# Performance work log

Hardware: AMD Instinct MI355X
Metric: run time of the kernel (lower is better)

Reference implementation:

```python
import jax, jax.numpy as jnp
from jax import lax
import numpy as np

SEARCH = 9          # search window (asserted == 9 in source)
PAD = SEARCH // 2   # 4
NUM_BINS = 10       # num_dist_bins
BIN_DISP = 0.5      # bin_displacement
NUM_ITER = 3        # num_iter
MIN_FILTER_REG = 1e-5


def _distance_map():
    # DistanceMap: soft-bin the radial distance from the window center.
    c = float(SEARCH // 2)
    yy, xx = jnp.meshgrid(jnp.arange(SEARCH, dtype=jnp.float32),
                          jnp.arange(SEARCH, dtype=jnp.float32), indexing='ij')
    d = jnp.sqrt((yy - c) ** 2 + (xx - c) ** 2) / BIN_DISP          # (9,9)
    k = jnp.arange(NUM_BINS, dtype=jnp.float32)
    bd = d[..., None] - k                                            # (9,9,B)
    vals = jnp.maximum(1.0 - jnp.abs(bd), 0.0)
    last = jnp.clip(bd[..., -1] + 1.0, 0.0, 1.0)                     # saturating last bin
    return vals.at[..., -1].set(last)                                # (9,9,B)


def _local_corr(f, ref_pad, disp):
    # f: (b,c,H,W); ref_pad: (b,c,H+8,W+8) -> scores (b,81,H,W)
    b, c, H, W = f.shape
    def step(_, d):
        r = lax.dynamic_slice(ref_pad, (0, 0, d[0], d[1]), (b, c, H, W))
        return None, jnp.einsum('bchw,bchw->bhw', f, r)
    _, out = lax.scan(step, None, disp)                              # (81,b,H,W)
    return jnp.moveaxis(out, 0, 1)


def _local_corr_t(res, ref_pad, disp):
    # res: (b,81,H,W) -> (b,c,H,W); adjoint of _local_corr w.r.t. the filter arg
    b, c = ref_pad.shape[0], ref_pad.shape[1]
    H, W = res.shape[2], res.shape[3]
    def step(acc, xs):
        d, rd = xs                                                   # rd: (b,H,W)
        r = lax.dynamic_slice(ref_pad, (0, 0, d[0], d[1]), (b, c, H, W))
        return acc + rd[:, None] * r, None
    acc0 = jnp.zeros((b, c, H, W), ref_pad.dtype)
    acc, _ = lax.scan(step, acc0, (disp, jnp.moveaxis(res, 1, 0)))
    return acc


def setup_inputs() -> dict:
    key = jax.random.key(0)
    k1, k2 = jax.random.split(key)
    b, c, H, W = 4, 128, 128, 128
    d = jnp.arange(NUM_BINS, dtype=jnp.float32) * BIN_DISP
    return {
        'filter_map': jax.random.normal(k1, (b, c, H, W), jnp.float32),
        'reference_feat': jax.random.normal(k2, (b, c, H, W), jnp.float32),
        # 1x1-conv predictor weights (num_bins -> 1), at their documented inits:
        'label_w': jnp.exp(-0.5 * d ** 2),            # init_gauss, sigma=1.0
        'spatial_w': jnp.ones((NUM_BINS,), jnp.float32),
        'mask_w': 4.0 * jnp.tanh(2.0 - d),            # v_minus_init_factor * tanh(2 - d)
        'log_step_length': jnp.zeros((1,), jnp.float32),   # log(1.0)
        'filter_reg': 0.01 * jnp.ones((1,), jnp.float32),
    }


def reference(filter_map, reference_feat, label_w, spatial_w, mask_w,
              log_step_length, filter_reg):
    b, c, H, W = filter_map.shape
    dm = _distance_map()                                             # (9,9,B)
    target_map = (dm @ label_w).reshape(1, SEARCH * SEARCH, 1, 1)
    v_plus = (dm @ spatial_w).reshape(1, SEARCH * SEARCH, 1, 1)
    weight_m = jax.nn.sigmoid(dm @ mask_w).reshape(1, SEARCH * SEARCH, 1, 1)

    step_length = jnp.exp(log_step_length).reshape(1, 1, 1, 1)
    reg_weight = jnp.maximum(filter_reg * filter_reg,
                             MIN_FILTER_REG ** 2).reshape(1, 1, 1, 1) / (c * c)

    dys, dxs = jnp.meshgrid(jnp.arange(SEARCH), jnp.arange(SEARCH), indexing='ij')
    disp = jnp.stack([dys.ravel(), dxs.ravel()], axis=1)             # (81,2)
    ref_pad = jnp.pad(reference_feat, ((0, 0), (0, 0), (PAD, PAD), (PAD, PAD)))

    # LeakyReluPar: f(s,a) = (1-a)/2*|s| + (1+a)/2*s ; deriv: (1-a)/2*sign(s) + (1+a)/2
    a_lo = (1.0 - weight_m) * 0.5
    a_hi = (1.0 + weight_m) * 0.5

    f = filter_map
    for _ in range(NUM_ITER):
        scores = _local_corr(f, ref_pad, disp)                       # (b,81,H,W)
        act = v_plus * (a_lo * jnp.abs(scores) + a_hi * scores)
        grad_act = v_plus * (a_lo * jnp.sign(scores) + a_hi)
        residuals = act - v_plus * target_map
        mapped = grad_act * residuals
        f_grad = reg_weight * f + _local_corr_t(mapped, ref_pad, disp)
        sg = grad_act * _local_corr(f_grad, ref_pad, disp)
        alpha_den = jnp.sum(sg * sg, axis=1, keepdims=True)          # (b,1,H,W)
        alpha_num = jnp.sum(f_grad * f_grad, axis=1, keepdims=True)
        alpha = alpha_num / jnp.maximum(alpha_den + reg_weight * alpha_num, 1e-8)
        f = f - step_length * alpha * f_grad
    return f
```

## Files before the change

### kernel.cpp

```cpp
#include <hip/hip_runtime.h>

#define BB 4
#define CC 128
#define HH 128
#define WW 128
#define HW (HH*WW)
#define CHW (CC*HW)
#define ND 81
#define CP 136
#define UPITCH 40
#define PP 32
#define SP 88

typedef short s8v __attribute__((ext_vector_type(8)));
typedef short s4v __attribute__((ext_vector_type(4)));
typedef float f4v __attribute__((ext_vector_type(4)));

__device__ __forceinline__ short f2bf(float x){
  unsigned u = __float_as_uint(x);
  unsigned r = (u + 0x7FFFu + ((u >> 16) & 1u)) >> 16;
  return (short)r;
}
__device__ __forceinline__ float bf2f(short s){
  return __uint_as_float(((unsigned)(unsigned short)s) << 16);
}

__global__ void coef_kernel(const float* lw, const float* sw, const float* mw,
                            const float* lsl, const float* fr, float* coef){
  int d = threadIdx.x;
  if (d < ND){
    float dy = (float)(d / 9) - 4.0f;
    float dx = (float)(d % 9) - 4.0f;
    float dist = sqrtf(dy*dy + dx*dx) * 2.0f;
    float t = 0.f, v = 0.f, m = 0.f;
    for (int k = 0; k < 10; k++){
      float bd = dist - (float)k;
      float val = (k == 9) ? fminf(fmaxf(bd + 1.0f, 0.f), 1.f)
                           : fmaxf(1.0f - fabsf(bd), 0.f);
      t += val * lw[k]; v += val * sw[k]; m += val * mw[k];
    }
    float wm = 1.f / (1.f + expf(-m));
    coef[d] = t; coef[128+d] = v;
    coef[256+d] = (1.f - wm) * 0.5f;
    coef[384+d] = (1.f + wm) * 0.5f;
  }
  if (threadIdx.x == 0){
    coef[512] = expf(lsl[0]);
    float f = fr[0];
    coef[513] = fmaxf(f*f, 1e-10f) / (float)(CC*CC);
  }
}

__global__ __launch_bounds__(256)
void cvt_kernel(const float* ref, short* refT, short* refU){
  __shared__ short T[128*130];
  int r = blockIdx.x, bb = blockIdx.y;
  int tid = threadIdx.x;
  const float* src = ref + (size_t)bb*CHW + (size_t)r*WW;
  short* uout = refU + (size_t)(bb*HH + r) * CC * WW;
  short* tout = refT + (size_t)(bb*HH + r) * WW * CC;
  #pragma unroll
  for (int k = 0; k < 16; k++){
    int q = tid + (k << 8);
    int c = q >> 5, u0 = (q & 31) * 4;
    float4 v = *(const float4*)(src + (size_t)c*HW + u0);
    short h0 = f2bf(v.x), h1 = f2bf(v.y), h2 = f2bf(v.z), h3 = f2bf(v.w);
    s4v pk = {h0, h1, h2, h3};
    *(s4v*)&uout[(size_t)c*WW + u0] = pk;
    T[c*130 + u0 + 0] = h0; T[c*130 + u0 + 1] = h1;
    T[c*130 + u0 + 2] = h2; T[c*130 + u0 + 3] = h3;
  }
  __syncthreads();
  #pragma unroll
  for (int k = 0; k < 16; k++){
    int o = tid + (k << 8);
    int u = o >> 5, c0 = (o & 31) * 4;
    s4v pk = {T[(c0+0)*130 + u], T[(c0+1)*130 + u],
              T[(c0+2)*130 + u], T[(c0+3)*130 + u]};
    *(s4v*)&tout[(size_t)u*CC + c0] = pk;
  }
}

#define L_UC   0
#define L_FGS  8704
#define L_CU   8704
#define L_PM   18944
#define L_CF   26112
#define L_SGN  27648
#define L_DEN  33280
#define L_NUM  33536
#define L_SA   33792
#define L_SZ   34048

template<int PRE>
__global__ __launch_bounds__(256, 4)
void kF(const float* f_in, const float* ref, const short* refT, const short* refU,
        const float* coef, float* f_out){
  __shared__ char smem[L_SZ];
  short* uc  = (short*)(smem + L_UC);
  short* cu  = (short*)(smem + L_CU);
  short* Pm  = (short*)(smem + L_PM);
  short* fgs = (short*)(smem + L_FGS);
  float* s_t = (float*)(smem + L_CF);
  float* s_v = s_t + 96; float* s_al = s_t + 192; float* s_ah = s_t + 288;
  signed char* sgn = (signed char*)(smem + L_SGN);
  float* den = (float*)(smem + L_DEN);
  float* num = (float*)(smem + L_NUM);
  float* sa  = (float*)(smem + L_SA);

  int tid = threadIdx.x;
  int lane = tid & 63, wv = tid >> 6;
  int quad = lane >> 4, col = lane & 15;

  int hwid = blockIdx.x + (blockIdx.y << 3) + (blockIdx.z << 8);
  int virt = ((hwid & 7) << 7) + (hwid >> 3);
  int bb = virt >> 8, y0 = ((virt >> 3) & 31) * 4, x0 = (virt & 7) * 16;

  int ub = x0 - 8;

  const float* fimg = f_in + (size_t)bb * CHW;
  const float* rimg = ref  + (size_t)bb * CHW;

  if (tid < ND){
    s_t[tid]  = coef[tid];       s_v[tid]  = coef[128+tid];
    s_al[tid] = coef[256+tid];   s_ah[tid] = coef[384+tid];
  }

  s8v pT0, pT1, pU0, pU1;
  float4 pF0, pF1, pF2, pF3;

  auto loadT = [&](int r){
    if constexpr (PRE){
      const short* tb = refT + (size_t)(bb*HH + r) * WW * CC;
      { int e = tid;       int ua = ub + (e >> 4);
        pT0 = (ua >= 0 && ua < WW)
              ? *(const s8v*)(tb + (size_t)ua*CC + ((e & 15) << 3)) : (s8v)(short)0; }
      { int e = tid + 256; int ua = ub + (e >> 4);
        pT1 = (ua >= 0 && ua < WW)
              ? *(const s8v*)(tb + (size_t)ua*CC + ((e & 15) << 3)) : (s8v)(short)0; }
    } else {
      const float* rb = rimg + (size_t)r * WW;
      float4 z; z.x = z.y = z.z = z.w = 0.f;
      { int e = tid;       int ua = ub + (e & 7)*4;
        pF0 = (ua >= 0 && ua + 4 <= WW) ? *(const float4*)(rb + (size_t)(e >> 3)*HW + ua) : z; }
      { int e = tid + 256; int ua = ub + (e & 7)*4;
        pF1 = (ua >= 0 && ua + 4 <= WW) ? *(const float4*)(rb + (size_t)(e >> 3)*HW + ua) : z; }
      { int e = tid + 512; int ua = ub + (e & 7)*4;
        pF2 = (ua >= 0 && ua + 4 <= WW) ? *(const float4*)(rb + (size_t)(e >> 3)*HW + ua) : z; }
      { int e = tid + 768; int ua = ub + (e & 7)*4;
        pF3 = (ua >= 0 && ua + 4 <= WW) ? *(const float4*)(rb + (size_t)(e >> 3)*HW + ua) : z; }
    }
  };
  auto loadU = [&](int r){
    if constexpr (PRE){
      const short* ubp = refU + (size_t)(bb*HH + r) * CC * WW;
      { int e = tid;       int ua = ub + ((e & 3) << 3);
        pU0 = (ua >= 0 && ua + 8 <= WW)
              ? *(const s8v*)(ubp + (size_t)(e >> 2)*WW + ua) : (s8v)(short)0; }
      { int e = tid + 256; int ua = ub + ((e & 3) << 3);
        pU1 = (ua >= 0 && ua + 8 <= WW)
              ? *(const s8v*)(ubp + (size_t)(e >> 2)*WW + ua) : (s8v)(short)0; }
    }
  };
  auto writeRowA = [&](){
    if constexpr (PRE){
      { int e = tid;       *(s8v*)&uc[(e >> 4)*CP + ((e & 15) << 3)] = pT0; }
      { int e = tid + 256; *(s8v*)&uc[(e >> 4)*CP + ((e & 15) << 3)] = pT1; }
      { int e = tid;       *(s8v*)&cu[(e >> 2)*UPITCH + ((e & 3) << 3)] = pU0; }
      { int e = tid + 256; *(s8v*)&cu[(e >> 2)*UPITCH + ((e & 3) << 3)] = pU1; }
    } else {
      float4 vv[4] = {pF0, pF1, pF2, pF3};
      #pragma unroll
      for (int k = 0; k < 4; k++){
        int e4 = tid + (k << 8);
        int u4 = (e4 & 7) * 4, c = e4 >> 3;
        short h0 = f2bf(vv[k].x), h1 = f2bf(vv[k].y),
              h2 = f2bf(vv[k].z), h3 = f2bf(vv[k].w);
        uc[(u4+0)*CP + c] = h0; uc[(u4+1)*CP + c] = h1;
        uc[(u4+2)*CP + c] = h2; uc[(u4+3)*CP + c] = h3;
        s4v pk = {h0, h1, h2, h3};
        *(s4v*)&cu[c*UPITCH + u4] = pk;
      }
    }
  };
  auto writeRowB = [&](){
    if constexpr (PRE){
      { int e = tid;       *(s8v*)&uc[(e >> 4)*CP + ((e & 15) << 3)] = pT0; }
      { int e = tid + 256; *(s8v*)&uc[(e >> 4)*CP + ((e & 15) << 3)] = pT1; }
    } else {
      float4 vv[4] = {pF0, pF1, pF2, pF3};
      #pragma unroll
      for (int k = 0; k < 4; k++){
        int e4 = tid + (k << 8);
        int u4 = (e4 & 7) * 4, c = e4 >> 3;
        uc[(u4+0)*CP + c] = f2bf(vv[k].x); uc[(u4+1)*CP + c] = f2bf(vv[k].y);
        uc[(u4+2)*CP + c] = f2bf(vv[k].z); uc[(u4+3)*CP + c] = f2bf(vv[k].w);
      }
    }
  };

  if (y0 - 4 >= 0){ loadT(y0 - 4); loadU(y0 - 4); }

  int fy = y0 + wv;
  s8v a_hi[4], a_lo[4];
  #pragma unroll
  for (int kc = 0; kc < 4; kc++){
    short th[8], tl[8];
    #pragma unroll
    for (int j = 0; j < 8; j++){
      int c = kc*32 + quad*8 + j;
      float v = fimg[(size_t)c * HW + fy * WW + x0 + col];
      short h = f2bf(v);
      th[j] = h; tl[j] = f2bf(v - bf2f(h));
    }
    a_hi[kc] = *(const s8v*)th;
    a_lo[kc] = *(const s8v*)tl;
  }

  f4v D[8];
  #pragma unroll
  for (int i = 0; i < 8; i++) D[i] = (f4v)0.f;

  for (int rr = 0; rr < 12; rr++){
    int r = y0 + rr - 4;
    bool rv = (r >= 0) && (r < HH);
    __syncthreads();
    if (rv) writeRowA();
    __syncthreads();
    if (rr < 11){
      int rn = r + 1;
      if (rn >= 0 && rn < HH){ loadT(rn); loadU(rn); }
    }
    int dy = rr - wv;
    if (rv && dy >= 0 && dy <= 8){
      f4v C0 = (f4v)0.f, C1 = (f4v)0.f;
      #pragma unroll
      for (int kc = 0; kc < 4; kc++){
        s8v b0 = *(const s8v*)&uc[col*CP      + kc*32 + quad*8];
        s8v b1 = *(const s8v*)&uc[(16+col)*CP + kc*32 + quad*8];
        C0 = __builtin_amdgcn_mfma_f32_16x16x32_bf16(a_hi[kc], b0, C0, 0,0,0);
        C0 = __builtin_amdgcn_mfma_f32_16x16x32_bf16(a_lo[kc], b0, C0, 0,0,0);
        C1 = __builtin_amdgcn_mfma_f32_16x16x32_bf16(a_hi[kc], b1, C1, 0,0,0);
        C1 = __builtin_amdgcn_mfma_f32_16x16x32_bf16(a_lo[kc], b1, C1, 0,0,0);
      }
      #pragma unroll
      for (int nt = 0; nt < 2; nt++){
        f4v Cv = nt ? C1 : C0;
        #pragma unroll
        for (int reg = 0; reg < 4; reg++){
          int x  = quad*4 + reg;
          int up = nt*16 + col;
          int dxm = up - x - 4;
          float m = 0.f;
          if (dxm >= 0 && dxm <= 8){
            float s = Cv[reg];
            int d = dy*9 + dxm;
            int px = wv*16 + x;
            signed char sc = (s > 0.f) ? (signed char)1
                           : ((s < 0.f) ? (signed char)-1 : (signed char)0);
            sgn[px*SP + d] = sc;
            float sgf = (float)sc;
            float vp = s_v[d], al = s_al[d], ah = s_ah[d];
            float ga  = vp * (al * sgf + ah);
            float act = vp * (al * fabsf(s) + ah * s);
            m = ga * (act - vp * s_t[d]);
          }
          Pm[(wv*16 + x)*PP + up] = f2bf(m);
        }
      }
      asm volatile("s_waitcnt lgkmcnt(0)" ::: "memory");
      __builtin_amdgcn_sched_barrier(0);
      s8v pa = *(const s8v*)&Pm[(wv*16 + col)*PP + quad*8];
      #pragma unroll
      for (int ct = 0; ct < 8; ct++){
        s8v bc = *(const s8v*)&cu[(ct*16 + col)*UPITCH + quad*8];
        D[ct] = __builtin_amdgcn_mfma_f32_16x16x32_bf16(pa, bc, D[ct], 0,0,0);
      }
    }
  }

  if (y0 - 4 >= 0) loadT(y0 - 4);

  float rw = coef[513];
  __syncthreads();
  #pragma unroll
  for (int ct = 0; ct < 8; ct++){
    #pragma unroll
    for (int reg = 0; reg < 4; reg++){
      int x = quad*4 + reg, c = ct*16 + col;
      float fv = fimg[(size_t)c * HW + fy * WW + x0 + x];
      fgs[(wv*16 + x)*CP + c] = f2bf(D[ct][reg] + rw * fv);
    }
  }
  __syncthreads();
  if (tid < 64){
    float s = 0.f;
    #pragma unroll
    for (int kc = 0; kc < 16; kc++){
      s8v v = *(const s8v*)&fgs[tid*CP + kc*8];
      #pragma unroll
      for (int j = 0; j < 8; j++){ float f = bf2f(v[j]); s += f*f; }
    }
    num[tid] = s;
  }

  s8v ga_[4];
  #pragma unroll
  for (int kc = 0; kc < 4; kc++)
    ga_[kc] = *(const s8v*)&fgs[(wv*16 + col)*CP + kc*32 + quad*8];

  float dacc[4] = {0.f, 0.f, 0.f, 0.f};

  for (int rr = 0; rr < 12; rr++){
    int r = y0 + rr - 4;
    bool rv = (r >= 0) && (r < HH);
    __syncthreads();
    if (rv) writeRowB();
    __syncthreads();
    if (rr < 11){
      int rn = r + 1;
      if (rn >= 0 && rn < HH) loadT(rn);
    }
    int dy = rr - wv;
    if (rv && dy >= 0 && dy <= 8){
      f4v C0 = (f4v)0.f, C1 = (f4v)0.f;
      #pragma unroll
      for (int kc = 0; kc < 4; kc++){
        s8v b0 = *(const s8v*)&uc[col*CP      + kc*32 + quad*8];
        s8v b1 = *(const s8v*)&uc[(16+col)*CP + kc*32 + quad*8];
        C0 = __builtin_amdgcn_mfma_f32_16x16x32_bf16(ga_[kc], b0, C0, 0,0,0);
        C1 = __builtin_amdgcn_mfma_f32_16x16x32_bf16(ga_[kc], b1, C1, 0,0,0);
      }
      #pragma unroll
      for (int nt = 0; nt < 2; nt++){
        f4v Cv = nt ? C1 : C0;
        #pragma unroll
        for (int reg = 0; reg < 4; reg++){
          int x  = quad*4 + reg;
          int up = nt*16 + col;
          int dxm = up - x - 4;
          if (dxm >= 0 && dxm <= 8){
            int d = dy*9 + dxm;
            int px = wv*16 + x;
            float sgf = (float)sgn[px*SP + d];
            float ga = s_v[d] * (s_al[d]*sgf + s_ah[d]);
            float t  = Cv[reg];
            float sgv = ga * t;
            dacc[reg] += sgv*sgv;
          }
        }
      }
    }
  }

  #pragma unroll
  for (int reg = 0; reg < 4; reg++){
    float v = dacc[reg];
    v += __shfl_xor(v, 1);
    v += __shfl_xor(v, 2);
    v += __shfl_xor(v, 4);
    v += __shfl_xor(v, 8);
    if (col == 0) den[wv*16 + quad*4 + reg] = v;
  }

  __syncthreads();
  if (tid < 64){
    float step = coef[512];
    float alpha = num[tid] / fmaxf(den[tid] + rw*num[tid], 1e-8f);
    sa[tid] = step * alpha;
  }
  __syncthreads();

  float* oimg = f_out + (size_t)bb * CHW;
  for (int e = tid; e < 8192; e += 256){
    int x = e & 15, y = (e >> 4) & 3, c = e >> 6;
    size_t gi = (size_t)c * HW + (y0 + y) * WW + x0 + x;
    float v = fimg[gi] - sa[y*16 + x] * bf2f(fgs[(y*16 + x)*CP + c]);
    oimg[gi] = v;
  }
}

extern "C" void kernel_launch(void* const* d_in, const int* in_sizes, int n_in,
                              void* d_out, int out_size, void* d_ws, size_t ws_size,
                              hipStream_t stream) {
  const float* filter_map = (const float*)d_in[0];
  const float* ref        = (const float*)d_in[1];
  const float* label_w    = (const float*)d_in[2];
  const float* spatial_w  = (const float*)d_in[3];
  const float* mask_w     = (const float*)d_in[4];
  const float* lsl        = (const float*)d_in[5];
  const float* freg       = (const float*)d_in[6];

  float* coef = (float*)d_ws;
  float* fbuf = (float*)d_out;

  short* refT = (short*)((char*)d_ws + 65536);
  short* refU = refT + (size_t)BB * CHW;
  size_t need = 65536 + 2 * (size_t)BB * CHW * sizeof(short);
  bool pre = (ws_size >= need);

  coef_kernel<<<dim3(1), dim3(128), 0, stream>>>(label_w, spatial_w, mask_w, lsl, freg, coef);
  if (pre)
    cvt_kernel<<<dim3(HH, BB), dim3(256), 0, stream>>>(ref, refT, refU);

  dim3 grid(8, 32, BB);
  for (int it = 0; it < 3; it++){
    const float* fsrc = (it == 0) ? filter_map : (const float*)fbuf;
    if (pre) kF<1><<<grid, 256, 0, stream>>>(fsrc, ref, refT, refU, coef, fbuf);
    else     kF<0><<<grid, 256, 0, stream>>>(fsrc, ref, refT, refU, coef, fbuf);
  }
}
```

Baseline: 351.7 us.

## Double-buffer reference rows, keep score signs in registers, fold activation coefficients

Row staging buffers in shared memory become double-buffered, so each iteration needs one barrier instead of two, and the next row is written while the current one is computed. Score signs move from a shared-memory byte array into packed 64-bit shift registers carried from the first sweep to the second. The per-displacement coefficients are pre-combined into three sign-selected gradient factors plus v*t, which simplifies the per-element math. The larger shared footprint drops launch bounds from 4 to 3 blocks per CU, trading occupancy for fewer syncs.

```diff
diff --git a/kernel.cpp b/kernel.cpp
--- a/kernel.cpp
+++ b/kernel.cpp
@@ -10,7 +10,8 @@
 #define CP 136
 #define UPITCH 40
 #define PP 32
-#define SP 88
+#define UCSZ (32*CP)
+#define CUSZ (128*UPITCH)
 
 typedef short s8v __attribute__((ext_vector_type(8)));
 typedef short s4v __attribute__((ext_vector_type(4)));
@@ -40,9 +41,10 @@
       t += val * lw[k]; v += val * sw[k]; m += val * mw[k];
     }
     float wm = 1.f / (1.f + expf(-m));
-    coef[d] = t; coef[128+d] = v;
-    coef[256+d] = (1.f - wm) * 0.5f;
-    coef[384+d] = (1.f + wm) * 0.5f;
+    coef[d]     = v;
+    coef[96+d]  = v * wm;
+    coef[192+d] = v * (1.f + wm) * 0.5f;
+    coef[288+d] = v * t;
   }
   if (threadIdx.x == 0){
     coef[512] = expf(lsl[0]);
@@ -82,18 +84,17 @@
 }
 
 #define L_UC   0
-#define L_FGS  8704
-#define L_CU   8704
-#define L_PM   18944
-#define L_CF   26112
-#define L_SGN  27648
-#define L_DEN  33280
-#define L_NUM  33536
-#define L_SA   33792
-#define L_SZ   34048
+#define L_CU   17408
+#define L_FGS  17408
+#define L_PM   37888
+#define L_CF   41984
+#define L_DEN  43520
+#define L_NUM  43776
+#define L_SA   44032
+#define L_SZ   44288
 
 template<int PRE>
-__global__ __launch_bounds__(256, 4)
+__global__ __launch_bounds__(256, 3)
 void kF(const float* f_in, const float* ref, const short* refT, const short* refU,
         const float* coef, float* f_out){
   __shared__ char smem[L_SZ];
@@ -101,9 +102,9 @@
   short* cu  = (short*)(smem + L_CU);
   short* Pm  = (short*)(smem + L_PM);
   short* fgs = (short*)(smem + L_FGS);
-  float* s_t = (float*)(smem + L_CF);
-  float* s_v = s_t + 96; float* s_al = s_t + 192; float* s_ah = s_t + 288;
-  signed char* sgn = (signed char*)(smem + L_SGN);
+  float* s_cf = (float*)(smem + L_CF);
+  float* s_vp = s_cf; float* s_vpwm = s_cf + 96;
+  float* s_vpah = s_cf + 192; float* s_vpt = s_cf + 288;
   float* den = (float*)(smem + L_DEN);
   float* num = (float*)(smem + L_NUM);
   float* sa  = (float*)(smem + L_SA);
@@ -120,11 +121,6 @@
 
   const float* fimg = f_in + (size_t)bb * CHW;
   const float* rimg = ref  + (size_t)bb * CHW;
-
-  if (tid < ND){
-    s_t[tid]  = coef[tid];       s_v[tid]  = coef[128+tid];
-    s_al[tid] = coef[256+tid];   s_ah[tid] = coef[384+tid];
-  }
 
   s8v pT0, pT1, pU0, pU1;
   float4 pF0, pF1, pF2, pF3;
@@ -162,12 +158,13 @@
               ? *(const s8v*)(ubp + (size_t)(e >> 2)*WW + ua) : (s8v)(short)0; }
     }
   };
-  auto writeRowA = [&](){
+  auto writeRowA = [&](int b){
+    short* ucb = uc + b*UCSZ; short* cub = cu + b*CUSZ;
     if constexpr (PRE){
-      { int e = tid;       *(s8v*)&uc[(e >> 4)*CP + ((e & 15) << 3)] = pT0; }
-      { int e = tid + 256; *(s8v*)&uc[(e >> 4)*CP + ((e & 15) << 3)] = pT1; }
-      { int e = tid;       *(s8v*)&cu[(e >> 2)*UPITCH + ((e & 3) << 3)] = pU0; }
-      { int e = tid + 256; *(s8v*)&cu[(e >> 2)*UPITCH + ((e & 3) << 3)] = pU1; }
+      { int e = tid;       *(s8v*)&ucb[(e >> 4)*CP + ((e & 15) << 3)] = pT0; }
+      { int e = tid + 256; *(s8v*)&ucb[(e >> 4)*CP + ((e & 15) << 3)] = pT1; }
+      { int e = tid;       *(s8v*)&cub[(e >> 2)*UPITCH + ((e & 3) << 3)] = pU0; }
+      { int e = tid + 256; *(s8v*)&cub[(e >> 2)*UPITCH + ((e & 3) << 3)] = pU1; }
     } else {
       float4 vv[4] = {pF0, pF1, pF2, pF3};
       #pragma unroll
@@ -176,30 +173,33 @@
         int u4 = (e4 & 7) * 4, c = e4 >> 3;
         short h0 = f2bf(vv[k].x), h1 = f2bf(vv[k].y),
               h2 = f2bf(vv[k].z), h3 = f2bf(vv[k].w);
-        uc[(u4+0)*CP + c] = h0; uc[(u4+1)*CP + c] = h1;
-        uc[(u4+2)*CP + c] = h2; uc[(u4+3)*CP + c] = h3;
+        ucb[(u4+0)*CP + c] = h0; ucb[(u4+1)*CP + c] = h1;
+        ucb[(u4+2)*CP + c] = h2; ucb[(u4+3)*CP + c] = h3;
         s4v pk = {h0, h1, h2, h3};
-        *(s4v*)&cu[c*UPITCH + u4] = pk;
+        *(s4v*)&cub[c*UPITCH + u4] = pk;
       }
     }
   };
-  auto writeRowB = [&](){
+  auto writeRowB = [&](int b){
+    short* ucb = uc + b*UCSZ;
     if constexpr (PRE){
-      { int e = tid;       *(s8v*)&uc[(e >> 4)*CP + ((e & 15) << 3)] = pT0; }
-      { int e = tid + 256; *(s8v*)&uc[(e >> 4)*CP + ((e & 15) << 3)] = pT1; }
+      { int e = tid;       *(s8v*)&ucb[(e >> 4)*CP + ((e & 15) << 3)] = pT0; }
+      { int e = tid + 256; *(s8v*)&ucb[(e >> 4)*CP + ((e & 15) << 3)] = pT1; }
     } else {
       float4 vv[4] = {pF0, pF1, pF2, pF3};
       #pragma unroll
       for (int k = 0; k < 4; k++){
         int e4 = tid + (k << 8);
         int u4 = (e4 & 7) * 4, c = e4 >> 3;
-        uc[(u4+0)*CP + c] = f2bf(vv[k].x); uc[(u4+1)*CP + c] = f2bf(vv[k].y);
-        uc[(u4+2)*CP + c] = f2bf(vv[k].z); uc[(u4+3)*CP + c] = f2bf(vv[k].w);
+        ucb[(u4+0)*CP + c] = f2bf(vv[k].x); ucb[(u4+1)*CP + c] = f2bf(vv[k].y);
+        ucb[(u4+2)*CP + c] = f2bf(vv[k].z); ucb[(u4+3)*CP + c] = f2bf(vv[k].w);
       }
     }
   };
 
   if (y0 - 4 >= 0){ loadT(y0 - 4); loadU(y0 - 4); }
+
+  for (int e = tid; e < 384; e += 256) s_cf[e] = coef[e];
 
   int fy = y0 + wv;
   s8v a_hi[4], a_lo[4];
@@ -221,61 +221,67 @@
   #pragma unroll
   for (int i = 0; i < 8; i++) D[i] = (f4v)0.f;
 
+  unsigned long long f0 = 0ull, f1 = 0ull, f2 = 0ull;
+
+  if (y0 - 4 >= 0) writeRowA(0);
+  if (y0 - 3 >= 0){ loadT(y0 - 3); loadU(y0 - 3); }
+
   for (int rr = 0; rr < 12; rr++){
     int r = y0 + rr - 4;
     bool rv = (r >= 0) && (r < HH);
     __syncthreads();
-    if (rv) writeRowA();
-    __syncthreads();
-    if (rr < 11){
-      int rn = r + 1;
-      if (rn >= 0 && rn < HH){ loadT(rn); loadU(rn); }
-    }
+    if (rr < 11 && r + 1 >= 0 && r + 1 < HH) writeRowA((rr + 1) & 1);
+    if (rr < 10 && r + 2 >= 0 && r + 2 < HH){ loadT(r + 2); loadU(r + 2); }
     int dy = rr - wv;
-    if (rv && dy >= 0 && dy <= 8){
-      f4v C0 = (f4v)0.f, C1 = (f4v)0.f;
-      #pragma unroll
-      for (int kc = 0; kc < 4; kc++){
-        s8v b0 = *(const s8v*)&uc[col*CP      + kc*32 + quad*8];
-        s8v b1 = *(const s8v*)&uc[(16+col)*CP + kc*32 + quad*8];
-        C0 = __builtin_amdgcn_mfma_f32_16x16x32_bf16(a_hi[kc], b0, C0, 0,0,0);
-        C0 = __builtin_amdgcn_mfma_f32_16x16x32_bf16(a_lo[kc], b0, C0, 0,0,0);
-        C1 = __builtin_amdgcn_mfma_f32_16x16x32_bf16(a_hi[kc], b1, C1, 0,0,0);
-        C1 = __builtin_amdgcn_mfma_f32_16x16x32_bf16(a_lo[kc], b1, C1, 0,0,0);
-      }
-      #pragma unroll
-      for (int nt = 0; nt < 2; nt++){
-        f4v Cv = nt ? C1 : C0;
+    if (dy >= 0 && dy <= 8){
+      unsigned pack = 0u;
+      if (rv){
+        const short* ucb = uc + (rr & 1)*UCSZ;
+        const short* cub = cu + (rr & 1)*CUSZ;
+        f4v C0 = (f4v)0.f, C1 = (f4v)0.f;
         #pragma unroll
-        for (int reg = 0; reg < 4; reg++){
-          int x  = quad*4 + reg;
-          int up = nt*16 + col;
-          int dxm = up - x - 4;
-          float m = 0.f;
-          if (dxm >= 0 && dxm <= 8){
-            float s = Cv[reg];
-            int d = dy*9 + dxm;
-            int px = wv*16 + x;
-            signed char sc = (s > 0.f) ? (signed char)1
-                           : ((s < 0.f) ? (signed char)-1 : (signed char)0);
-            sgn[px*SP + d] = sc;
-            float sgf = (float)sc;
-            float vp = s_v[d], al = s_al[d], ah = s_ah[d];
-            float ga  = vp * (al * sgf + ah);
-            float act = vp * (al * fabsf(s) + ah * s);
-            m = ga * (act - vp * s_t[d]);
+        for (int kc = 0; kc < 4; kc++){
+          s8v b0 = *(const s8v*)&ucb[col*CP      + kc*32 + quad*8];
+          s8v b1 = *(const s8v*)&ucb[(16+col)*CP + kc*32 + quad*8];
+          C0 = __builtin_amdgcn_mfma_f32_16x16x32_bf16(a_hi[kc], b0, C0, 0,0,0);
+          C0 = __builtin_amdgcn_mfma_f32_16x16x32_bf16(a_lo[kc], b0, C0, 0,0,0);
+          C1 = __builtin_amdgcn_mfma_f32_16x16x32_bf16(a_hi[kc], b1, C1, 0,0,0);
+          C1 = __builtin_amdgcn_mfma_f32_16x16x32_bf16(a_lo[kc], b1, C1, 0,0,0);
+        }
+        #pragma unroll
+        for (int nt = 0; nt < 2; nt++){
+          f4v Cv = nt ? C1 : C0;
+          #pragma unroll
+          for (int reg = 0; reg < 4; reg++){
+            int x  = quad*4 + reg;
+            int up = nt*16 + col;
+            int dxm = up - x - 4;
+            float m = 0.f;
+            if ((unsigned)dxm <= 8u){
+              float s = Cv[reg];
+              int d = dy*9 + dxm;
+              unsigned pos = (s > 0.f) ? 1u : 0u;
+              unsigned neg = (s < 0.f) ? 1u : 0u;
+              const float* gap = pos ? s_vp : (neg ? s_vpwm : s_vpah);
+              float ga = gap[d];
+              m = ga * (ga * s - s_vpt[d]);
+              pack |= (pos | (neg << 1)) << ((nt*4 + reg) * 2);
+            }
+            Pm[(wv*16 + x)*PP + up] = f2bf(m);
           }
-          Pm[(wv*16 + x)*PP + up] = f2bf(m);
+        }
+        asm volatile("s_waitcnt lgkmcnt(0)" ::: "memory");
+        __builtin_amdgcn_sched_barrier(0);
+        s8v pa = *(const s8v*)&Pm[(wv*16 + col)*PP + quad*8];
+        #pragma unroll
+        for (int ct = 0; ct < 8; ct++){
+          s8v bc = *(const s8v*)&cub[(ct*16 + col)*UPITCH + quad*8];
+          D[ct] = __builtin_amdgcn_mfma_f32_16x16x32_bf16(pa, bc, D[ct], 0,0,0);
         }
       }
-      asm volatile("s_waitcnt lgkmcnt(0)" ::: "memory");
-      __builtin_amdgcn_sched_barrier(0);
-      s8v pa = *(const s8v*)&Pm[(wv*16 + col)*PP + quad*8];
-      #pragma unroll
-      for (int ct = 0; ct < 8; ct++){
-        s8v bc = *(const s8v*)&cu[(ct*16 + col)*UPITCH + quad*8];
-        D[ct] = __builtin_amdgcn_mfma_f32_16x16x32_bf16(pa, bc, D[ct], 0,0,0);
-      }
+      f0 = (f0 >> 16) | (f1 << 48);
+      f1 = (f1 >> 16) | (f2 << 48);
+      f2 = (f2 >> 16) | ((unsigned long long)pack << 48);
     }
   }
 
@@ -309,44 +315,49 @@
   for (int kc = 0; kc < 4; kc++)
     ga_[kc] = *(const s8v*)&fgs[(wv*16 + col)*CP + kc*32 + quad*8];
 
+  if (y0 - 4 >= 0) writeRowB(0);
+  if (y0 - 3 >= 0) loadT(y0 - 3);
+
   float dacc[4] = {0.f, 0.f, 0.f, 0.f};
 
   for (int rr = 0; rr < 12; rr++){
     int r = y0 + rr - 4;
     bool rv = (r >= 0) && (r < HH);
     __syncthreads();
-    if (rv) writeRowB();
-    __syncthreads();
-    if (rr < 11){
-      int rn = r + 1;
-      if (rn >= 0 && rn < HH) loadT(rn);
-    }
+    if (rr < 11 && r + 1 >= 0 && r + 1 < HH) writeRowB((rr + 1) & 1);
+    if (rr < 10 && r + 2 >= 0 && r + 2 < HH) loadT(r + 2);
     int dy = rr - wv;
-    if (rv && dy >= 0 && dy <= 8){
-      f4v C0 = (f4v)0.f, C1 = (f4v)0.f;
-      #pragma unroll
-      for (int kc = 0; kc < 4; kc++){
-        s8v b0 = *(const s8v*)&uc[col*CP      + kc*32 + quad*8];
-        s8v b1 = *(const s8v*)&uc[(16+col)*CP + kc*32 + quad*8];
-        C0 = __builtin_amdgcn_mfma_f32_16x16x32_bf16(ga_[kc], b0, C0, 0,0,0);
-        C1 = __builtin_amdgcn_mfma_f32_16x16x32_bf16(ga_[kc], b1, C1, 0,0,0);
-      }
-      #pragma unroll
-      for (int nt = 0; nt < 2; nt++){
-        f4v Cv = nt ? C1 : C0;
+    if (dy >= 0 && dy <= 8){
+      unsigned pack = (unsigned)(f0 >> 48) & 0xFFFFu;
+      f0 = (f0 >> 16) | (f1 << 48);
+      f1 = (f1 >> 16) | (f2 << 48);
+      f2 >>= 16;
+      if (rv){
+        const short* ucb = uc + (rr & 1)*UCSZ;
+        f4v C0 = (f4v)0.f, C1 = (f4v)0.f;
         #pragma unroll
-        for (int reg = 0; reg < 4; reg++){
-          int x  = quad*4 + reg;
-          int up = nt*16 + col;
-          int dxm = up - x - 4;
-          if (dxm >= 0 && dxm <= 8){
-            int d = dy*9 + dxm;
-            int px = wv*16 + x;
-            float sgf = (float)sgn[px*SP + d];
-            float ga = s_v[d] * (s_al[d]*sgf + s_ah[d]);
-            float t  = Cv[reg];
-            float sgv = ga * t;
-            dacc[reg] += sgv*sgv;
+        for (int kc = 0; kc < 4; kc++){
+          s8v b0 = *(const s8v*)&ucb[col*CP      + kc*32 + quad*8];
+          s8v b1 = *(const s8v*)&ucb[(16+col)*CP + kc*32 + quad*8];
+          C0 = __builtin_amdgcn_mfma_f32_16x16x32_bf16(ga_[kc], b0, C0, 0,0,0);
+          C1 = __builtin_amdgcn_mfma_f32_16x16x32_bf16(ga_[kc], b1, C1, 0,0,0);
+        }
+        #pragma unroll
+        for (int nt = 0; nt < 2; nt++){
+          f4v Cv = nt ? C1 : C0;
+          #pragma unroll
+          for (int reg = 0; reg < 4; reg++){
+            int x  = quad*4 + reg;
+            int up = nt*16 + col;
+            int dxm = up - x - 4;
+            if ((unsigned)dxm <= 8u){
+              int d = dy*9 + dxm;
+              unsigned b2 = pack >> ((nt*4 + reg) * 2);
+              const float* gap = (b2 & 1u) ? s_vp : ((b2 & 2u) ? s_vpwm : s_vpah);
+              float ga = gap[d];
+              float sgv = ga * Cv[reg];
+              dacc[reg] += sgv*sgv;
+            }
           }
         }
       }
```

Result: slower. 388.0 us (+10.3%).

## Precompute sign-indexed coefficient tables and keep score signs in registers

Applied to the files above, without the earlier changes.

The coefficient kernel now precomputes, for each of the three score-sign cases, the squared gradient factor and its product with the target. The residual-times-gradient term therefore collapses to a single fma, and the denominator term uses one table lookup. The per-pixel sign array in shared memory is removed. The signs are packed as 2-bit fields into three 64-bit registers that shift like a queue from the first pass to the second, which cuts LDS traffic and shared-memory footprint. The cost is extra register pressure, plus reliance on the shift sequence of both loops matching exactly.

```diff
diff --git a/kernel.cpp b/kernel.cpp
--- a/kernel.cpp
+++ b/kernel.cpp
@@ -10,7 +10,6 @@
 #define CP 136
 #define UPITCH 40
 #define PP 32
-#define SP 88
 
 typedef short s8v __attribute__((ext_vector_type(8)));
 typedef short s4v __attribute__((ext_vector_type(4)));
@@ -40,14 +39,20 @@
       t += val * lw[k]; v += val * sw[k]; m += val * mw[k];
     }
     float wm = 1.f / (1.f + expf(-m));
-    coef[d] = t; coef[128+d] = v;
-    coef[256+d] = (1.f - wm) * 0.5f;
-    coef[384+d] = (1.f + wm) * 0.5f;
+    float ah = (1.f + wm) * 0.5f;
+    float gp = v, gn = v * wm, gz = v * ah;
+    float vt = v * t;
+    coef[d]       = gp * gp;
+    coef[96+d]    = gn * gn;
+    coef[192+d]   = gz * gz;
+    coef[288+d]   = gp * vt;
+    coef[384+d]   = gn * vt;
+    coef[480+d]   = gz * vt;
   }
   if (threadIdx.x == 0){
-    coef[512] = expf(lsl[0]);
+    coef[576] = expf(lsl[0]);
     float f = fr[0];
-    coef[513] = fmaxf(f*f, 1e-10f) / (float)(CC*CC);
+    coef[577] = fmaxf(f*f, 1e-10f) / (float)(CC*CC);
   }
 }
 
@@ -86,11 +91,10 @@
 #define L_CU   8704
 #define L_PM   18944
 #define L_CF   26112
-#define L_SGN  27648
-#define L_DEN  33280
-#define L_NUM  33536
-#define L_SA   33792
-#define L_SZ   34048
+#define L_DEN  28672
+#define L_NUM  28928
+#define L_SA   29184
+#define L_SZ   29440
 
 template<int PRE>
 __global__ __launch_bounds__(256, 4)
@@ -101,9 +105,9 @@
   short* cu  = (short*)(smem + L_CU);
   short* Pm  = (short*)(smem + L_PM);
   short* fgs = (short*)(smem + L_FGS);
-  float* s_t = (float*)(smem + L_CF);
-  float* s_v = s_t + 96; float* s_al = s_t + 192; float* s_ah = s_t + 288;
-  signed char* sgn = (signed char*)(smem + L_SGN);
+  float* s_cf = (float*)(smem + L_CF);
+  float* s_g2 = s_cf;
+  float* s_gt = s_cf + 288;
   float* den = (float*)(smem + L_DEN);
   float* num = (float*)(smem + L_NUM);
   float* sa  = (float*)(smem + L_SA);
@@ -120,11 +124,6 @@
 
   const float* fimg = f_in + (size_t)bb * CHW;
   const float* rimg = ref  + (size_t)bb * CHW;
-
-  if (tid < ND){
-    s_t[tid]  = coef[tid];       s_v[tid]  = coef[128+tid];
-    s_al[tid] = coef[256+tid];   s_ah[tid] = coef[384+tid];
-  }
 
   s8v pT0, pT1, pU0, pU1;
   float4 pF0, pF1, pF2, pF3;
@@ -201,6 +200,8 @@
 
   if (y0 - 4 >= 0){ loadT(y0 - 4); loadU(y0 - 4); }
 
+  for (int e = tid; e < 640; e += 256) s_cf[e] = coef[e];
+
   int fy = y0 + wv;
   s8v a_hi[4], a_lo[4];
   #pragma unroll
@@ -220,6 +221,8 @@
   f4v D[8];
   #pragma unroll
   for (int i = 0; i < 8; i++) D[i] = (f4v)0.f;
+
+  unsigned long long f0 = 0ull, f1 = 0ull, f2 = 0ull;
 
   for (int rr = 0; rr < 12; rr++){
     int r = y0 + rr - 4;
@@ -232,56 +235,60 @@
       if (rn >= 0 && rn < HH){ loadT(rn); loadU(rn); }
     }
     int dy = rr - wv;
-    if (rv && dy >= 0 && dy <= 8){
-      f4v C0 = (f4v)0.f, C1 = (f4v)0.f;
-      #pragma unroll
-      for (int kc = 0; kc < 4; kc++){
-        s8v b0 = *(const s8v*)&uc[col*CP      + kc*32 + quad*8];
-        s8v b1 = *(const s8v*)&uc[(16+col)*CP + kc*32 + quad*8];
-        C0 = __builtin_amdgcn_mfma_f32_16x16x32_bf16(a_hi[kc], b0, C0, 0,0,0);
-        C0 = __builtin_amdgcn_mfma_f32_16x16x32_bf16(a_lo[kc], b0, C0, 0,0,0);
-        C1 = __builtin_amdgcn_mfma_f32_16x16x32_bf16(a_hi[kc], b1, C1, 0,0,0);
-        C1 = __builtin_amdgcn_mfma_f32_16x16x32_bf16(a_lo[kc], b1, C1, 0,0,0);
-      }
-      #pragma unroll
-      for (int nt = 0; nt < 2; nt++){
-        f4v Cv = nt ? C1 : C0;
+    if (dy >= 0 && dy <= 8){
+      unsigned pack = 0u;
+      if (rv){
+        f4v C0 = (f4v)0.f, C1 = (f4v)0.f;
         #pragma unroll
-        for (int reg = 0; reg < 4; reg++){
-          int x  = quad*4 + reg;
-          int up = nt*16 + col;
-          int dxm = up - x - 4;
-          float m = 0.f;
-          if (dxm >= 0 && dxm <= 8){
-            float s = Cv[reg];
-            int d = dy*9 + dxm;
-            int px = wv*16 + x;
-            signed char sc = (s > 0.f) ? (signed char)1
-                           : ((s < 0.f) ? (signed char)-1 : (signed char)0);
-            sgn[px*SP + d] = sc;
-            float sgf = (float)sc;
-            float vp = s_v[d], al = s_al[d], ah = s_ah[d];
-            float ga  = vp * (al * sgf + ah);
-            float act = vp * (al * fabsf(s) + ah * s);
-            m = ga * (act - vp * s_t[d]);
+        for (int kc = 0; kc < 4; kc++){
+          s8v b0 = *(const s8v*)&uc[col*CP      + kc*32 + quad*8];
+          s8v b1 = *(const s8v*)&uc[(16+col)*CP + kc*32 + quad*8];
+          C0 = __builtin_amdgcn_mfma_f32_16x16x32_bf16(a_hi[kc], b0, C0, 0,0,0);
+          C0 = __builtin_amdgcn_mfma_f32_16x16x32_bf16(a_lo[kc], b0, C0, 0,0,0);
+          C1 = __builtin_amdgcn_mfma_f32_16x16x32_bf16(a_hi[kc], b1, C1, 0,0,0);
+          C1 = __builtin_amdgcn_mfma_f32_16x16x32_bf16(a_lo[kc], b1, C1, 0,0,0);
+        }
+        #pragma unroll
+        for (int nt = 0; nt < 2; nt++){
+          f4v Cv = nt ? C1 : C0;
+          #pragma unroll
+          for (int reg = 0; reg < 4; reg++){
+            int x  = quad*4 + reg;
+            int up = nt*16 + col;
+            int dxm = up - x - 4;
+            float m = 0.f;
+            if ((unsigned)dxm <= 8u){
+              float s = Cv[reg];
+              int d = dy*9 + dxm;
+              unsigned pos = (s > 0.f) ? 1u : 0u;
+              unsigned neg = (s < 0.f) ? 1u : 0u;
+              int off = pos ? 0 : (neg ? 96 : 192);
+              float g2 = s_g2[off + d];
+              float gt = s_gt[off + d];
+              m = fmaf(g2, s, -gt);
+              pack |= (pos | (neg << 1)) << ((nt*4 + reg) * 2);
+            }
+            Pm[(wv*16 + x)*PP + up] = f2bf(m);
           }
-          Pm[(wv*16 + x)*PP + up] = f2bf(m);
+        }
+        asm volatile("s_waitcnt lgkmcnt(0)" ::: "memory");
+        __builtin_amdgcn_sched_barrier(0);
+        s8v pa = *(const s8v*)&Pm[(wv*16 + col)*PP + quad*8];
+        #pragma unroll
+        for (int ct = 0; ct < 8; ct++){
+          s8v bc = *(const s8v*)&cu[(ct*16 + col)*UPITCH + quad*8];
+          D[ct] = __builtin_amdgcn_mfma_f32_16x16x32_bf16(pa, bc, D[ct], 0,0,0);
         }
       }
-      asm volatile("s_waitcnt lgkmcnt(0)" ::: "memory");
-      __builtin_amdgcn_sched_barrier(0);
-      s8v pa = *(const s8v*)&Pm[(wv*16 + col)*PP + quad*8];
-      #pragma unroll
-      for (int ct = 0; ct < 8; ct++){
-        s8v bc = *(const s8v*)&cu[(ct*16 + col)*UPITCH + quad*8];
-        D[ct] = __builtin_amdgcn_mfma_f32_16x16x32_bf16(pa, bc, D[ct], 0,0,0);
-      }
+      f0 = (f0 >> 16) | (f1 << 48);
+      f1 = (f1 >> 16) | (f2 << 48);
+      f2 = (f2 >> 16) | ((unsigned long long)pack << 48);
     }
   }
 
   if (y0 - 4 >= 0) loadT(y0 - 4);
 
-  float rw = coef[513];
+  float rw = s_cf[577];
   __syncthreads();
   #pragma unroll
   for (int ct = 0; ct < 8; ct++){
@@ -322,31 +329,36 @@
       if (rn >= 0 && rn < HH) loadT(rn);
     }
     int dy = rr - wv;
-    if (rv && dy >= 0 && dy <= 8){
-      f4v C0 = (f4v)0.f, C1 = (f4v)0.f;
-      #pragma unroll
-      for (int kc = 0; kc < 4; kc++){
-        s8v b0 = *(const s8v*)&uc[col*CP      + kc*32 + quad*8];
-        s8v b1 = *(const s8v*)&uc[(16+col)*CP + kc*32 + quad*8];
-        C0 = __builtin_amdgcn_mfma_f32_16x16x32_bf16(ga_[kc], b0, C0, 0,0,0);
-        C1 = __builtin_amdgcn_mfma_f32_16x16x32_bf16(ga_[kc], b1, C1, 0,0,0);
-      }
-      #pragma unroll
-      for (int nt = 0; nt < 2; nt++){
-        f4v Cv = nt ? C1 : C0;
+    if (dy >= 0 && dy <= 8){
+      unsigned pack = (unsigned)(f0 >> 48) & 0xFFFFu;
+      f0 = (f0 >> 16) | (f1 << 48);
+      f1 = (f1 >> 16) | (f2 << 48);
+      f2 >>= 16;
+      if (rv){
+        f4v C0 = (f4v)0.f, C1 = (f4v)0.f;
         #pragma unroll
-        for (int reg = 0; reg < 4; reg++){
-          int x  = quad*4 + reg;
-          int up = nt*16 + col;
-          int dxm = up - x - 4;
-          if (dxm >= 0 && dxm <= 8){
-            int d = dy*9 + dxm;
-            int px = wv*16 + x;
-            float sgf = (float)sgn[px*SP + d];
-            float ga = s_v[d] * (s_al[d]*sgf + s_ah[d]);
-            float t  = Cv[reg];
-            float sgv = ga * t;
-            dacc[reg] += sgv*sgv;
+        for (int kc = 0; kc < 4; kc++){
+          s8v b0 = *(const s8v*)&uc[col*CP      + kc*32 + quad*8];
+          s8v b1 = *(const s8v*)&uc[(16+col)*CP + kc*32 + quad*8];
+          C0 = __builtin_amdgcn_mfma_f32_16x16x32_bf16(ga_[kc], b0, C0, 0,0,0);
+          C1 = __builtin_amdgcn_mfma_f32_16x16x32_bf16(ga_[kc], b1, C1, 0,0,0);
+        }
+        #pragma unroll
+        for (int nt = 0; nt < 2; nt++){
+          f4v Cv = nt ? C1 : C0;
+          #pragma unroll
+          for (int reg = 0; reg < 4; reg++){
+            int x  = quad*4 + reg;
+            int up = nt*16 + col;
+            int dxm = up - x - 4;
+            if ((unsigned)dxm <= 8u){
+              int d = dy*9 + dxm;
+              unsigned b2 = pack >> ((nt*4 + reg) * 2);
+              int off = (b2 & 1u) ? 0 : ((b2 & 2u) ? 96 : 192);
+              float g2 = s_g2[off + d];
+              float t  = Cv[reg];
+              dacc[reg] = fmaf(g2 * t, t, dacc[reg]);
+            }
           }
         }
       }
@@ -365,7 +377,7 @@
 
   __syncthreads();
   if (tid < 64){
-    float step = coef[512];
+    float step = s_cf[576];
     float alpha = num[tid] / fmaxf(den[tid] + rw*num[tid], 1e-8f);
     sa[tid] = step * alpha;
   }
```

New measurement: 335.5 us. 1.05x faster.
